# Optimization experiments

Hardware: AMD Instinct MI355X
Metric: run time of the kernel (lower is better)

The kernel has to match this reference:

```python
import jax, jax.numpy as jnp
import numpy as np

N_HEAD = 32
HEAD_DIM = 32  # must equal N_HEAD due to the module's einsum index reuse
N_EMBD = N_HEAD * HEAD_DIM
VOCAB = 32000
B, T = 2, 64
TEMP_MIN = 0.1


def setup_inputs() -> dict:
    key = jax.random.key(0)
    ks = jax.random.split(key, 8)
    inv = 1.0 / np.sqrt(HEAD_DIM)
    return {
        "x": jax.random.normal(ks[0], (B, T, N_EMBD), dtype=jnp.float32),
        "vocab_emb": jax.random.normal(ks[1], (VOCAB, N_EMBD), dtype=jnp.float32) * 0.02,
        "W_ffn": jax.random.normal(ks[2], (HEAD_DIM, HEAD_DIM), dtype=jnp.float32) * inv,
        "b_ffn": jnp.zeros((HEAD_DIM,), dtype=jnp.float32),
        "temps": jnp.ones((N_HEAD,), dtype=jnp.float32),
        "W_ref": jax.random.normal(ks[3], (HEAD_DIM, HEAD_DIM), dtype=jnp.float32) * inv,
        "b_ref": jnp.zeros((HEAD_DIM,), dtype=jnp.float32),
        "W_gate": jax.random.normal(ks[4], (HEAD_DIM, HEAD_DIM), dtype=jnp.float32) * inv,
        "b_gate": jnp.zeros((HEAD_DIM,), dtype=jnp.float32),
    }


def reference(x, vocab_emb, W_ffn, b_ffn, temps, W_ref, b_ref, W_gate, b_gate):
    Bs, Ts, C = x.shape
    # per-head channel decomposition: (B*T, n_head, head_dim)
    xc = x.reshape(Bs * Ts, N_HEAD, HEAD_DIM)
    # channel_ffns: shared Linear over the head_dim axis (torch Linear: x @ W.T + b)
    ffn = jnp.einsum('bnh,dh->bnd', xc, W_ffn) + b_ffn
    # vocab channels: (n_head, vocab, head_dim)
    vc = vocab_emb.reshape(VOCAB, N_HEAD, HEAD_DIM).transpose(1, 0, 2)
    temps_c = jnp.clip(temps, TEMP_MIN, None)[None, :, None]

    def vocab_project(q):
        # faithful to torch: einsum('bnh,hvd->bnv') contracts q's head_dim
        # against vc's HEAD axis and sums over d as well (requires head_dim == n_head)
        logits = jnp.einsum('bnh,hvd->bnv', q, vc)
        w = jax.nn.softmax(logits / temps_c, axis=-1)  # (B*T, n_head, vocab)
        return jnp.einsum('bnv,hvd->bnh', w, vc)

    vocab_out = vocab_project(ffn)  # (B*T, n_head, head_dim)

    # refinement stage (use_vocab_refinement=True)
    refinement = jnp.tanh(jnp.einsum('bnh,dh->bnd', xc, W_ref) + b_ref)
    gate = jax.nn.sigmoid(jnp.einsum('bnh,dh->bnd', xc, W_gate) + b_gate)
    refined = vocab_out * (1.0 - gate) + refinement * gate
    vocab_out = vocab_project(refined)

    # dropout p=0 (eval) -> identity
    return vocab_out.reshape(Bs, Ts, C)
```

## Files before the change

### kernel.cpp

```cpp
#include <hip/hip_runtime.h>
#include <hip/hip_bf16.h>
#include <cstdint>

typedef unsigned int uint;
typedef unsigned short ushort_t;

typedef __attribute__((ext_vector_type(8))) short short8;
typedef __attribute__((ext_vector_type(4))) short short4_t;
typedef __attribute__((ext_vector_type(4))) float float4_t;

#define NEMBD 1024
#define VOCAB 32000
#define LOG2E 1.4426950408889634f

__device__ __forceinline__ ushort_t f2bf_rne(float f) {
    uint u = __float_as_uint(f);
    u += 0x7fffu + ((u >> 16) & 1u);
    return (ushort_t)(u >> 16);
}

__global__ void k_build_st(const float* __restrict__ ve, ushort_t* __restrict__ ST) {
    int v = blockIdx.x;
    int t = threadIdx.x;
    const float4* row = (const float4*)(ve + (size_t)v * NEMBD);
    float4 f = row[t];
    float s = f.x + f.y + f.z + f.w;
    s += __shfl_down(s, 4, 8);
    s += __shfl_down(s, 2, 8);
    s += __shfl_down(s, 1, 8);
    if ((t & 7) == 0) ST[v * 32 + (t >> 3)] = f2bf_rne(s);
}

__global__ void k_build_s2(const ushort_t* __restrict__ ST, ushort_t* __restrict__ S2) {
    int tid = blockIdx.x * 256 + threadIdx.x;
    int l = tid & 63, f = (tid >> 6) & 1, c = tid >> 7;
    int quad = l >> 4, lo = l & 15;
    uint w[4];
    #pragma unroll
    for (int t = 0; t < 2; t++) {
        #pragma unroll
        for (int jj = 0; jj < 2; jj++) {
            ushort_t v0 = ST[(c * 32 + t * 16 + quad * 4 + jj * 2 + 0) * 32 + f * 16 + lo];
            ushort_t v1 = ST[(c * 32 + t * 16 + quad * 4 + jj * 2 + 1) * 32 + f * 16 + lo];
            w[t * 2 + jj] = (uint)v0 | ((uint)v1 << 16);
        }
    }
    uint4* dst = (uint4*)S2;
    dst[tid] = make_uint4(w[0], w[1], w[2], w[3]);
}

__global__ void k_q1(const float* __restrict__ x, const float* __restrict__ W,
                     const float* __restrict__ b, const float* __restrict__ temps,
                     ushort_t* __restrict__ q1) {
    int tid = blockIdx.x * 256 + threadIdx.x;
    int i = tid >> 5, d = tid & 31, n = i & 31;
    const float* xr = x + i * 32;
    float s = b[d];
    #pragma unroll
    for (int h = 0; h < 32; h++) s += xr[h] * W[d * 32 + h];
    q1[tid] = f2bf_rne(s * (LOG2E / fmaxf(temps[n], 0.1f)));
}

__launch_bounds__(256, 4)
__global__ void k_proj(const ushort_t* __restrict__ ST, const ushort_t* __restrict__ S2,
                       const ushort_t* __restrict__ q, float* __restrict__ pN,
                       float* __restrict__ pD) {
    int g = blockIdx.x >> 4, p = blockIdx.x & 15;
    int wave = threadIdx.x >> 6, lane = threadIdx.x & 63;
    int quad = lane >> 4, lo = lane & 15;

    short8 qf[4];
    #pragma unroll
    for (int s = 0; s < 4; s++)
        qf[s] = *(const short8*)(q + ((g * 64 + s * 16 + lo) * 32 + quad * 8));

    float4_t pv0[4], pv1[4];
    float dsum[4];
    #pragma unroll
    for (int s = 0; s < 4; s++) {
        pv0[s] = (float4_t){0.f, 0.f, 0.f, 0.f};
        pv1[s] = (float4_t){0.f, 0.f, 0.f, 0.f};
        dsum[s] = 0.f;
    }
    const float4_t zero4 = (float4_t){0.f, 0.f, 0.f, 0.f};

    int start = (p * 125) >> 1, end = ((p + 1) * 125) >> 1;
    for (int k = start + wave; k < end; k += 4) {
        const ushort_t* pa = ST + ((k * 32 + lo) * 32 + quad * 8);
        short8 a0 = *(const short8*)pa;
        short8 a1 = *(const short8*)(pa + 512);
        const ushort_t* pb = S2 + ((size_t)(k * 2) * 64 + lane) * 8;
        short8 sb0 = *(const short8*)pb;
        short8 sb1 = *(const short8*)(pb + 512);
        short4_t b00 = {sb0[0], sb0[1], sb0[2], sb0[3]};
        short4_t b01 = {sb0[4], sb0[5], sb0[6], sb0[7]};
        short4_t b10 = {sb1[0], sb1[1], sb1[2], sb1[3]};
        short4_t b11 = {sb1[4], sb1[5], sb1[6], sb1[7]};

        #pragma unroll
        for (int s = 0; s < 4; s++) {
            float4_t l0 = __builtin_amdgcn_mfma_f32_16x16x32_bf16(a0, qf[s], zero4, 0, 0, 0);
            float4_t l1 = __builtin_amdgcn_mfma_f32_16x16x32_bf16(a1, qf[s], zero4, 0, 0, 0);
            float e0 = __builtin_amdgcn_exp2f(l0[0]);
            float e1 = __builtin_amdgcn_exp2f(l0[1]);
            float e2 = __builtin_amdgcn_exp2f(l0[2]);
            float e3 = __builtin_amdgcn_exp2f(l0[3]);
            float f0 = __builtin_amdgcn_exp2f(l1[0]);
            float f1 = __builtin_amdgcn_exp2f(l1[1]);
            float f2 = __builtin_amdgcn_exp2f(l1[2]);
            float f3 = __builtin_amdgcn_exp2f(l1[3]);
            uint u0 = __builtin_amdgcn_perm(__float_as_uint(e1), __float_as_uint(e0), 0x07060302u);
            uint u1 = __builtin_amdgcn_perm(__float_as_uint(e3), __float_as_uint(e2), 0x07060302u);
            uint u2 = __builtin_amdgcn_perm(__float_as_uint(f1), __float_as_uint(f0), 0x07060302u);
            uint u3 = __builtin_amdgcn_perm(__float_as_uint(f3), __float_as_uint(f2), 0x07060302u);
            dsum[s] += __uint_as_float(u0 << 16) + __uint_as_float(u0 & 0xffff0000u)
                     + __uint_as_float(u1 << 16) + __uint_as_float(u1 & 0xffff0000u)
                     + __uint_as_float(u2 << 16) + __uint_as_float(u2 & 0xffff0000u)
                     + __uint_as_float(u3 << 16) + __uint_as_float(u3 & 0xffff0000u);
            union { uint u[2]; short4_t s4; } c0, c1;
            c0.u[0] = u0; c0.u[1] = u1;
            c1.u[0] = u2; c1.u[1] = u3;
            short4_t P0 = c0.s4, P1 = c1.s4;
            pv0[s] = __builtin_amdgcn_mfma_f32_16x16x16bf16_1k(P0, b00, pv0[s], 0, 0, 0);
            pv0[s] = __builtin_amdgcn_mfma_f32_16x16x16bf16_1k(P1, b01, pv0[s], 0, 0, 0);
            pv1[s] = __builtin_amdgcn_mfma_f32_16x16x16bf16_1k(P0, b10, pv1[s], 0, 0, 0);
            pv1[s] = __builtin_amdgcn_mfma_f32_16x16x16bf16_1k(P1, b11, pv1[s], 0, 0, 0);
        }
    }

    #pragma unroll
    for (int s = 0; s < 4; s++) {
        dsum[s] += __shfl_xor(dsum[s], 16, 64);
        dsum[s] += __shfl_xor(dsum[s], 32, 64);
    }

    __shared__ float red[4][64][9];
    int gp = blockIdx.x;
    for (int s = 0; s < 4; s++) {
        #pragma unroll
        for (int r = 0; r < 4; r++) {
            red[wave][lane][r]     = pv0[s][r];
            red[wave][lane][4 + r] = pv1[s][r];
        }
        red[wave][lane][8] = dsum[s];
        __syncthreads();
        if (wave == 0) {
            #pragma unroll
            for (int r = 0; r < 4; r++) {
                float n0 = 0.f, n1 = 0.f;
                #pragma unroll
                for (int w = 0; w < 4; w++) {
                    n0 += red[w][lane][r];
                    n1 += red[w][lane][4 + r];
                }
                int ql = s * 16 + quad * 4 + r;
                pN[((size_t)gp * 64 + ql) * 32 + lo]      = n0;
                pN[((size_t)gp * 64 + ql) * 32 + 16 + lo] = n1;
            }
            if (quad == 0) {
                float dd = red[0][lane][8] + red[1][lane][8] + red[2][lane][8] + red[3][lane][8];
                pD[gp * 64 + s * 16 + lo] = dd;
            }
        }
        __syncthreads();
    }
}

__global__ void k_refine(const float* __restrict__ pN, const float* __restrict__ pD,
                         const float* __restrict__ x,
                         const float* __restrict__ Wr, const float* __restrict__ br,
                         const float* __restrict__ Wg, const float* __restrict__ bg,
                         const float* __restrict__ temps, ushort_t* __restrict__ q2) {
    int tid = blockIdx.x * 256 + threadIdx.x;
    int i = tid >> 5, h = tid & 31, n = i & 31;
    int g = i >> 6, ql = i & 63;
    float N = 0.f, D = 0.f;
    #pragma unroll
    for (int p = 0; p < 16; p++) {
        N += pN[((size_t)(g * 16 + p) * 64 + ql) * 32 + h];
        D += pD[(g * 16 + p) * 64 + ql];
    }
    float vo = N / D;
    const float* xr = x + i * 32;
    float sr = br[h], sg = bg[h];
    #pragma unroll
    for (int h2 = 0; h2 < 32; h2++) {
        sr += xr[h2] * Wr[h * 32 + h2];
        sg += xr[h2] * Wg[h * 32 + h2];
    }
    float ref  = tanhf(sr);
    float gate = 1.f / (1.f + __expf(-sg));
    float refined = vo * (1.f - gate) + ref * gate;
    q2[tid] = f2bf_rne(refined * (LOG2E / fmaxf(temps[n], 0.1f)));
}

__global__ void k_final(const float* __restrict__ pN, const float* __restrict__ pD,
                        float* __restrict__ out) {
    int tid = blockIdx.x * 256 + threadIdx.x;
    int i = tid >> 5, h = tid & 31;
    int g = i >> 6, ql = i & 63;
    float N = 0.f, D = 0.f;
    #pragma unroll
    for (int p = 0; p < 16; p++) {
        N += pN[((size_t)(g * 16 + p) * 64 + ql) * 32 + h];
        D += pD[(g * 16 + p) * 64 + ql];
    }
    out[tid] = N / D;
}

extern "C" void kernel_launch(void* const* d_in, const int* in_sizes, int n_in,
                              void* d_out, int out_size, void* d_ws, size_t ws_size,
                              hipStream_t stream) {
    const float* x     = (const float*)d_in[0];
    const float* ve    = (const float*)d_in[1];
    const float* Wf    = (const float*)d_in[2];
    const float* bf    = (const float*)d_in[3];
    const float* temps = (const float*)d_in[4];
    const float* Wr    = (const float*)d_in[5];
    const float* br    = (const float*)d_in[6];
    const float* Wg    = (const float*)d_in[7];
    const float* bg    = (const float*)d_in[8];
    float* out = (float*)d_out;

    char* ws = (char*)d_ws;
    ushort_t* ST = (ushort_t*)ws;
    ushort_t* S2 = (ushort_t*)(ws + 2048000);
    ushort_t* q1 = (ushort_t*)(ws + 4096000);
    ushort_t* q2 = (ushort_t*)(ws + 4096000 + 262144);
    float* pN = (float*)(ws + 4096000 + 2 * 262144);
    float* pD = (float*)(ws + 4096000 + 2 * 262144 + 8388608);

    k_build_st<<<dim3(VOCAB), dim3(256), 0, stream>>>(ve, ST);
    k_build_s2<<<dim3(500), dim3(256), 0, stream>>>(ST, S2);
    k_q1<<<dim3(512), dim3(256), 0, stream>>>(x, Wf, bf, temps, q1);
    k_proj<<<dim3(1024), dim3(256), 0, stream>>>(ST, S2, q1, pN, pD);
    k_refine<<<dim3(512), dim3(256), 0, stream>>>(pN, pD, x, Wr, br, Wg, bg, temps, q2);
    k_proj<<<dim3(1024), dim3(256), 0, stream>>>(ST, S2, q2, pN, pD);
    k_final<<<dim3(512), dim3(256), 0, stream>>>(pN, pD, out);
}
```

Baseline: 266.4 us.

## Fuse vocab build kernels and fold q-projection and refinement into projection kernels

Merges the two vocabulary preprocessing kernels into one block-per-32-rows kernel that builds both the ST and swizzled S2 layouts through shared memory. It also fuses the q1 projection into the first projection kernel and the refinement/gate step into the second, computing each block's 64 query rows into LDS. The aim is to cut kernel launches and the global round trips for q1/q2, and to remove the extra ST reread. In exchange, each of the 16 blocks sharing a query group recomputes the same small prologue, and the second stage now needs double-buffered partial arrays.

```diff
diff --git a/kernel.cpp b/kernel.cpp
--- a/kernel.cpp
+++ b/kernel.cpp
@@ -19,60 +19,80 @@
     return (ushort_t)(u >> 16);
 }
 
-__global__ void k_build_st(const float* __restrict__ ve, ushort_t* __restrict__ ST) {
-    int v = blockIdx.x;
+__global__ void k_build(const float* __restrict__ ve, ushort_t* __restrict__ ST,
+                        ushort_t* __restrict__ S2) {
+    int blk = blockIdx.x;
     int t = threadIdx.x;
-    const float4* row = (const float4*)(ve + (size_t)v * NEMBD);
-    float4 f = row[t];
-    float s = f.x + f.y + f.z + f.w;
-    s += __shfl_down(s, 4, 8);
-    s += __shfl_down(s, 2, 8);
-    s += __shfl_down(s, 1, 8);
-    if ((t & 7) == 0) ST[v * 32 + (t >> 3)] = f2bf_rne(s);
-}
-
-__global__ void k_build_s2(const ushort_t* __restrict__ ST, ushort_t* __restrict__ S2) {
-    int tid = blockIdx.x * 256 + threadIdx.x;
-    int l = tid & 63, f = (tid >> 6) & 1, c = tid >> 7;
-    int quad = l >> 4, lo = l & 15;
-    uint w[4];
-    #pragma unroll
-    for (int t = 0; t < 2; t++) {
-        #pragma unroll
-        for (int jj = 0; jj < 2; jj++) {
-            ushort_t v0 = ST[(c * 32 + t * 16 + quad * 4 + jj * 2 + 0) * 32 + f * 16 + lo];
-            ushort_t v1 = ST[(c * 32 + t * 16 + quad * 4 + jj * 2 + 1) * 32 + f * 16 + lo];
-            w[t * 2 + jj] = (uint)v0 | ((uint)v1 << 16);
-        }
-    }
-    uint4* dst = (uint4*)S2;
-    dst[tid] = make_uint4(w[0], w[1], w[2], w[3]);
-}
-
-__global__ void k_q1(const float* __restrict__ x, const float* __restrict__ W,
-                     const float* __restrict__ b, const float* __restrict__ temps,
-                     ushort_t* __restrict__ q1) {
-    int tid = blockIdx.x * 256 + threadIdx.x;
-    int i = tid >> 5, d = tid & 31, n = i & 31;
-    const float* xr = x + i * 32;
-    float s = b[d];
-    #pragma unroll
-    for (int h = 0; h < 32; h++) s += xr[h] * W[d * 32 + h];
-    q1[tid] = f2bf_rne(s * (LOG2E / fmaxf(temps[n], 0.1f)));
+    int r = t >> 5, h = t & 31;
+    const float4* src = (const float4*)(ve + ((size_t)(blk * 32 + r)) * NEMBD + h * 32);
+    float s = 0.f;
+    #pragma unroll
+    for (int j = 0; j < 8; j++) {
+        float4 f = src[j];
+        s += f.x + f.y + f.z + f.w;
+    }
+    __shared__ __align__(16) ushort_t sm[1024];
+    sm[r * 32 + h] = f2bf_rne(s);
+    __syncthreads();
+    if (t < 128) {
+        ((uint4*)(ST + blk * 1024))[t] = ((const uint4*)sm)[t];
+    } else if (t < 256) {
+        int tt = t - 128;
+        int l = tt & 63, f = tt >> 6;
+        int quad = l >> 4, lo = l & 15;
+        uint w[4];
+        #pragma unroll
+        for (int t2 = 0; t2 < 2; t2++) {
+            #pragma unroll
+            for (int jj = 0; jj < 2; jj++) {
+                ushort_t v0 = sm[(t2 * 16 + quad * 4 + jj * 2 + 0) * 32 + f * 16 + lo];
+                ushort_t v1 = sm[(t2 * 16 + quad * 4 + jj * 2 + 1) * 32 + f * 16 + lo];
+                w[t2 * 2 + jj] = (uint)v0 | ((uint)v1 << 16);
+            }
+        }
+        ((uint4*)(S2 + blk * 1024))[tt] = make_uint4(w[0], w[1], w[2], w[3]);
+    }
 }
 
 __launch_bounds__(256, 4)
-__global__ void k_proj(const ushort_t* __restrict__ ST, const ushort_t* __restrict__ S2,
-                       const ushort_t* __restrict__ q, float* __restrict__ pN,
-                       float* __restrict__ pD) {
+__global__ void k_proj1(const ushort_t* __restrict__ ST, const ushort_t* __restrict__ S2,
+                        const float* __restrict__ x, const float* __restrict__ Wf,
+                        const float* __restrict__ bfn, const float* __restrict__ temps,
+                        float* __restrict__ pN, float* __restrict__ pD) {
+    __shared__ __align__(16) ushort_t qs[64 * 32];
+    __shared__ float red[4][64][9];
     int g = blockIdx.x >> 4, p = blockIdx.x & 15;
-    int wave = threadIdx.x >> 6, lane = threadIdx.x & 63;
+    int t = threadIdx.x;
+    int wave = t >> 6, lane = t & 63;
     int quad = lane >> 4, lo = lane & 15;
 
+    {
+        int r = t >> 2, c4 = t & 3;
+        int i = g * 64 + r, n = i & 31;
+        float sc = LOG2E / fmaxf(temps[n], 0.1f);
+        const float4* xv4 = (const float4*)(x + (size_t)i * 32);
+        float4 xv[8];
+        #pragma unroll
+        for (int j = 0; j < 8; j++) xv[j] = xv4[j];
+        #pragma unroll
+        for (int jj = 0; jj < 8; jj++) {
+            int d = c4 * 8 + jj;
+            const float4* wr = (const float4*)(Wf + d * 32);
+            float s = bfn[d];
+            #pragma unroll
+            for (int j2 = 0; j2 < 8; j2++) {
+                float4 w = wr[j2], xx = xv[j2];
+                s += xx.x * w.x + xx.y * w.y + xx.z * w.z + xx.w * w.w;
+            }
+            qs[r * 32 + d] = f2bf_rne(s * sc);
+        }
+    }
+    __syncthreads();
+
     short8 qf[4];
     #pragma unroll
     for (int s = 0; s < 4; s++)
-        qf[s] = *(const short8*)(q + ((g * 64 + s * 16 + lo) * 32 + quad * 8));
+        qf[s] = *(const short8*)(qs + (s * 16 + lo) * 32 + quad * 8);
 
     float4_t pv0[4], pv1[4];
     float dsum[4];
@@ -134,7 +154,6 @@
         dsum[s] += __shfl_xor(dsum[s], 32, 64);
     }
 
-    __shared__ float red[4][64][9];
     int gp = blockIdx.x;
     for (int s = 0; s < 4; s++) {
         #pragma unroll
@@ -166,32 +185,161 @@
     }
 }
 
-__global__ void k_refine(const float* __restrict__ pN, const float* __restrict__ pD,
-                         const float* __restrict__ x,
-                         const float* __restrict__ Wr, const float* __restrict__ br,
-                         const float* __restrict__ Wg, const float* __restrict__ bg,
-                         const float* __restrict__ temps, ushort_t* __restrict__ q2) {
-    int tid = blockIdx.x * 256 + threadIdx.x;
-    int i = tid >> 5, h = tid & 31, n = i & 31;
-    int g = i >> 6, ql = i & 63;
-    float N = 0.f, D = 0.f;
-    #pragma unroll
-    for (int p = 0; p < 16; p++) {
-        N += pN[((size_t)(g * 16 + p) * 64 + ql) * 32 + h];
-        D += pD[(g * 16 + p) * 64 + ql];
-    }
-    float vo = N / D;
-    const float* xr = x + i * 32;
-    float sr = br[h], sg = bg[h];
-    #pragma unroll
-    for (int h2 = 0; h2 < 32; h2++) {
-        sr += xr[h2] * Wr[h * 32 + h2];
-        sg += xr[h2] * Wg[h * 32 + h2];
-    }
-    float ref  = tanhf(sr);
-    float gate = 1.f / (1.f + __expf(-sg));
-    float refined = vo * (1.f - gate) + ref * gate;
-    q2[tid] = f2bf_rne(refined * (LOG2E / fmaxf(temps[n], 0.1f)));
+__launch_bounds__(256, 4)
+__global__ void k_proj2(const ushort_t* __restrict__ ST, const ushort_t* __restrict__ S2,
+                        const float* __restrict__ pNa, const float* __restrict__ pDa,
+                        const float* __restrict__ x,
+                        const float* __restrict__ Wr, const float* __restrict__ br,
+                        const float* __restrict__ Wg, const float* __restrict__ bg,
+                        const float* __restrict__ temps,
+                        float* __restrict__ pN, float* __restrict__ pD) {
+    __shared__ __align__(16) ushort_t qs[64 * 32];
+    __shared__ float red[4][64][9];
+    int g = blockIdx.x >> 4, p = blockIdx.x & 15;
+    int t = threadIdx.x;
+    int wave = t >> 6, lane = t & 63;
+    int quad = lane >> 4, lo = lane & 15;
+
+    {
+        int r = t >> 2, c4 = t & 3;
+        int i = g * 64 + r, n = i & 31;
+        float sc = LOG2E / fmaxf(temps[n], 0.1f);
+        float4 N0 = make_float4(0.f, 0.f, 0.f, 0.f);
+        float4 N1 = make_float4(0.f, 0.f, 0.f, 0.f);
+        float D = 0.f;
+        #pragma unroll
+        for (int pp = 0; pp < 16; pp++) {
+            const float* base = pNa + (((size_t)(g * 16 + pp) * 64 + r) * 32 + c4 * 8);
+            float4 a = *(const float4*)base;
+            float4 b = *(const float4*)(base + 4);
+            N0.x += a.x; N0.y += a.y; N0.z += a.z; N0.w += a.w;
+            N1.x += b.x; N1.y += b.y; N1.z += b.z; N1.w += b.w;
+            D += pDa[(g * 16 + pp) * 64 + r];
+        }
+        float invD = 1.0f / D;
+        float vo[8] = {N0.x * invD, N0.y * invD, N0.z * invD, N0.w * invD,
+                       N1.x * invD, N1.y * invD, N1.z * invD, N1.w * invD};
+        const float4* xv4 = (const float4*)(x + (size_t)i * 32);
+        float4 xv[8];
+        #pragma unroll
+        for (int j = 0; j < 8; j++) xv[j] = xv4[j];
+        #pragma unroll
+        for (int jj = 0; jj < 8; jj++) {
+            int d = c4 * 8 + jj;
+            const float4* wrr = (const float4*)(Wr + d * 32);
+            const float4* wgg = (const float4*)(Wg + d * 32);
+            float sr = br[d], sg = bg[d];
+            #pragma unroll
+            for (int j2 = 0; j2 < 8; j2++) {
+                float4 w1 = wrr[j2], w2 = wgg[j2], xx = xv[j2];
+                sr += xx.x * w1.x + xx.y * w1.y + xx.z * w1.z + xx.w * w1.w;
+                sg += xx.x * w2.x + xx.y * w2.y + xx.z * w2.z + xx.w * w2.w;
+            }
+            sr = fminf(fmaxf(sr, -20.f), 20.f);
+            float tE = __builtin_amdgcn_exp2f(sr * (2.f * LOG2E));
+            float th = (tE - 1.f) * __builtin_amdgcn_rcpf(tE + 1.f);
+            float gE = __builtin_amdgcn_exp2f(fminf(fmaxf(-sg, -20.f), 20.f) * LOG2E);
+            float gate = __builtin_amdgcn_rcpf(1.f + gE);
+            float refined = vo[jj] + gate * (th - vo[jj]);
+            qs[r * 32 + d] = f2bf_rne(refined * sc);
+        }
+    }
+    __syncthreads();
+
+    short8 qf[4];
+    #pragma unroll
+    for (int s = 0; s < 4; s++)
+        qf[s] = *(const short8*)(qs + (s * 16 + lo) * 32 + quad * 8);
+
+    float4_t pv0[4], pv1[4];
+    float dsum[4];
+    #pragma unroll
+    for (int s = 0; s < 4; s++) {
+        pv0[s] = (float4_t){0.f, 0.f, 0.f, 0.f};
+        pv1[s] = (float4_t){0.f, 0.f, 0.f, 0.f};
+        dsum[s] = 0.f;
+    }
+    const float4_t zero4 = (float4_t){0.f, 0.f, 0.f, 0.f};
+
+    int start = (p * 125) >> 1, end = ((p + 1) * 125) >> 1;
+    for (int k = start + wave; k < end; k += 4) {
+        const ushort_t* pa = ST + ((k * 32 + lo) * 32 + quad * 8);
+        short8 a0 = *(const short8*)pa;
+        short8 a1 = *(const short8*)(pa + 512);
+        const ushort_t* pb = S2 + ((size_t)(k * 2) * 64 + lane) * 8;
+        short8 sb0 = *(const short8*)pb;
+        short8 sb1 = *(const short8*)(pb + 512);
+        short4_t b00 = {sb0[0], sb0[1], sb0[2], sb0[3]};
+        short4_t b01 = {sb0[4], sb0[5], sb0[6], sb0[7]};
+        short4_t b10 = {sb1[0], sb1[1], sb1[2], sb1[3]};
+        short4_t b11 = {sb1[4], sb1[5], sb1[6], sb1[7]};
+
+        #pragma unroll
+        for (int s = 0; s < 4; s++) {
+            float4_t l0 = __builtin_amdgcn_mfma_f32_16x16x32_bf16(a0, qf[s], zero4, 0, 0, 0);
+            float4_t l1 = __builtin_amdgcn_mfma_f32_16x16x32_bf16(a1, qf[s], zero4, 0, 0, 0);
+            float e0 = __builtin_amdgcn_exp2f(l0[0]);
+            float e1 = __builtin_amdgcn_exp2f(l0[1]);
+            float e2 = __builtin_amdgcn_exp2f(l0[2]);
+            float e3 = __builtin_amdgcn_exp2f(l0[3]);
+            float f0 = __builtin_amdgcn_exp2f(l1[0]);
+            float f1 = __builtin_amdgcn_exp2f(l1[1]);
+            float f2 = __builtin_amdgcn_exp2f(l1[2]);
+            float f3 = __builtin_amdgcn_exp2f(l1[3]);
+            uint u0 = __builtin_amdgcn_perm(__float_as_uint(e1), __float_as_uint(e0), 0x07060302u);
+            uint u1 = __builtin_amdgcn_perm(__float_as_uint(e3), __float_as_uint(e2), 0x07060302u);
+            uint u2 = __builtin_amdgcn_perm(__float_as_uint(f1), __float_as_uint(f0), 0x07060302u);
+            uint u3 = __builtin_amdgcn_perm(__float_as_uint(f3), __float_as_uint(f2), 0x07060302u);
+            dsum[s] += __uint_as_float(u0 << 16) + __uint_as_float(u0 & 0xffff0000u)
+                     + __uint_as_float(u1 << 16) + __uint_as_float(u1 & 0xffff0000u)
+                     + __uint_as_float(u2 << 16) + __uint_as_float(u2 & 0xffff0000u)
+                     + __uint_as_float(u3 << 16) + __uint_as_float(u3 & 0xffff0000u);
+            union { uint u[2]; short4_t s4; } c0, c1;
+            c0.u[0] = u0; c0.u[1] = u1;
+            c1.u[0] = u2; c1.u[1] = u3;
+            short4_t P0 = c0.s4, P1 = c1.s4;
+            pv0[s] = __builtin_amdgcn_mfma_f32_16x16x16bf16_1k(P0, b00, pv0[s], 0, 0, 0);
+            pv0[s] = __builtin_amdgcn_mfma_f32_16x16x16bf16_1k(P1, b01, pv0[s], 0, 0, 0);
+            pv1[s] = __builtin_amdgcn_mfma_f32_16x16x16bf16_1k(P0, b10, pv1[s], 0, 0, 0);
+            pv1[s] = __builtin_amdgcn_mfma_f32_16x16x16bf16_1k(P1, b11, pv1[s], 0, 0, 0);
+        }
+    }
+
+    #pragma unroll
+    for (int s = 0; s < 4; s++) {
+        dsum[s] += __shfl_xor(dsum[s], 16, 64);
+        dsum[s] += __shfl_xor(dsum[s], 32, 64);
+    }
+
+    int gp = blockIdx.x;
+    for (int s = 0; s < 4; s++) {
+        #pragma unroll
+        for (int r = 0; r < 4; r++) {
+            red[wave][lane][r]     = pv0[s][r];
+            red[wave][lane][4 + r] = pv1[s][r];
+        }
+        red[wave][lane][8] = dsum[s];
+        __syncthreads();
+        if (wave == 0) {
+            #pragma unroll
+            for (int r = 0; r < 4; r++) {
+                float n0 = 0.f, n1 = 0.f;
+                #pragma unroll
+                for (int w = 0; w < 4; w++) {
+                    n0 += red[w][lane][r];
+                    n1 += red[w][lane][4 + r];
+                }
+                int ql = s * 16 + quad * 4 + r;
+                pN[((size_t)gp * 64 + ql) * 32 + lo]      = n0;
+                pN[((size_t)gp * 64 + ql) * 32 + 16 + lo] = n1;
+            }
+            if (quad == 0) {
+                float dd = red[0][lane][8] + red[1][lane][8] + red[2][lane][8] + red[3][lane][8];
+                pD[gp * 64 + s * 16 + lo] = dd;
+            }
+        }
+        __syncthreads();
+    }
 }
 
 __global__ void k_final(const float* __restrict__ pN, const float* __restrict__ pD,
@@ -214,7 +362,7 @@
     const float* x     = (const float*)d_in[0];
     const float* ve    = (const float*)d_in[1];
     const float* Wf    = (const float*)d_in[2];
-    const float* bf    = (const float*)d_in[3];
+    const float* bfn   = (const float*)d_in[3];
     const float* temps = (const float*)d_in[4];
     const float* Wr    = (const float*)d_in[5];
     const float* br    = (const float*)d_in[6];
@@ -223,18 +371,16 @@
     float* out = (float*)d_out;
 
     char* ws = (char*)d_ws;
-    ushort_t* ST = (ushort_t*)ws;
-    ushort_t* S2 = (ushort_t*)(ws + 2048000);
-    ushort_t* q1 = (ushort_t*)(ws + 4096000);
-    ushort_t* q2 = (ushort_t*)(ws + 4096000 + 262144);
-    float* pN = (float*)(ws + 4096000 + 2 * 262144);
-    float* pD = (float*)(ws + 4096000 + 2 * 262144 + 8388608);
-
-    k_build_st<<<dim3(VOCAB), dim3(256), 0, stream>>>(ve, ST);
-    k_build_s2<<<dim3(500), dim3(256), 0, stream>>>(ST, S2);
-    k_q1<<<dim3(512), dim3(256), 0, stream>>>(x, Wf, bf, temps, q1);
-    k_proj<<<dim3(1024), dim3(256), 0, stream>>>(ST, S2, q1, pN, pD);
-    k_refine<<<dim3(512), dim3(256), 0, stream>>>(pN, pD, x, Wr, br, Wg, bg, temps, q2);
-    k_proj<<<dim3(1024), dim3(256), 0, stream>>>(ST, S2, q2, pN, pD);
-    k_final<<<dim3(512), dim3(256), 0, stream>>>(pN, pD, out);
-}
+    ushort_t* ST  = (ushort_t*)ws;
+    ushort_t* S2  = (ushort_t*)(ws + 2048000);
+    float* pNa = (float*)(ws + 4096000);
+    float* pDa = (float*)(ws + 4096000 + 8388608);
+    float* pNb = (float*)(ws + 4096000 + 8388608 + 262144);
+    float* pDb = (float*)(ws + 4096000 + 2 * 8388608 + 262144);
+
+    k_build<<<dim3(1000), dim3(1024), 0, stream>>>(ve, ST, S2);
+    k_proj1<<<dim3(1024), dim3(256), 0, stream>>>(ST, S2, x, Wf, bfn, temps, pNa, pDa);
+    k_proj2<<<dim3(1024), dim3(256), 0, stream>>>(ST, S2, pNa, pDa, x, Wr, br, Wg, bg,
+                                                  temps, pNb, pDb);
+    k_final<<<dim3(512), dim3(256), 0, stream>>>(pNb, pDb, out);
+}
```

New measurement: 343.8 us. +29.0%, slower.

## Stage vocab tiles in LDS shared across waves and split vocab finer

Applied to the files above, without the earlier changes.

The projection kernel now has all four waves share each vocab chunk. A new pack kernel pre-lays the chunks out, and they are double-buffered through LDS. Each wave owns one 16-row query slice instead of all four, which removes the cross-wave LDS reduction at the end. The vocab split goes from 16 to 32 partitions, so the grid doubles and the reduce kernels sum twice as many partials. This trades register pressure and redundant global loads for extra barriers, more partial-sum traffic and an extra packed copy of the table.

```diff
diff --git a/kernel.cpp b/kernel.cpp
--- a/kernel.cpp
+++ b/kernel.cpp
@@ -31,22 +31,31 @@
     if ((t & 7) == 0) ST[v * 32 + (t >> 3)] = f2bf_rne(s);
 }
 
-__global__ void k_build_s2(const ushort_t* __restrict__ ST, ushort_t* __restrict__ S2) {
-    int tid = blockIdx.x * 256 + threadIdx.x;
-    int l = tid & 63, f = (tid >> 6) & 1, c = tid >> 7;
-    int quad = l >> 4, lo = l & 15;
-    uint w[4];
-    #pragma unroll
-    for (int t = 0; t < 2; t++) {
+__global__ void k_pack(const ushort_t* __restrict__ ST, ushort_t* __restrict__ SA,
+                       ushort_t* __restrict__ S2) {
+    int c = blockIdx.x;
+    int t = threadIdx.x;
+    if (t < 128) {
+        int tile = t >> 6, lane = t & 63;
+        int quad = lane >> 4, lo = lane & 15;
+        uint4 d = *(const uint4*)(ST + ((size_t)(c * 32 + tile * 16 + lo)) * 32 + quad * 8);
+        ((uint4*)SA)[c * 128 + t] = d;
+    } else {
+        int tt = t - 128;
+        int f = tt >> 6, l = tt & 63;
+        int quad = l >> 4, lo = l & 15;
+        uint w[4];
         #pragma unroll
-        for (int jj = 0; jj < 2; jj++) {
-            ushort_t v0 = ST[(c * 32 + t * 16 + quad * 4 + jj * 2 + 0) * 32 + f * 16 + lo];
-            ushort_t v1 = ST[(c * 32 + t * 16 + quad * 4 + jj * 2 + 1) * 32 + f * 16 + lo];
-            w[t * 2 + jj] = (uint)v0 | ((uint)v1 << 16);
-        }
-    }
-    uint4* dst = (uint4*)S2;
-    dst[tid] = make_uint4(w[0], w[1], w[2], w[3]);
+        for (int t2 = 0; t2 < 2; t2++) {
+            #pragma unroll
+            for (int jj = 0; jj < 2; jj++) {
+                ushort_t v0 = ST[(c * 32 + t2 * 16 + quad * 4 + jj * 2 + 0) * 32 + f * 16 + lo];
+                ushort_t v1 = ST[(c * 32 + t2 * 16 + quad * 4 + jj * 2 + 1) * 32 + f * 16 + lo];
+                w[t2 * 2 + jj] = (uint)v0 | ((uint)v1 << 16);
+            }
+        }
+        ((uint4*)S2)[c * 128 + tt] = make_uint4(w[0], w[1], w[2], w[3]);
+    }
 }
 
 __global__ void k_q1(const float* __restrict__ x, const float* __restrict__ W,
@@ -61,46 +70,65 @@
     q1[tid] = f2bf_rne(s * (LOG2E / fmaxf(temps[n], 0.1f)));
 }
 
-__launch_bounds__(256, 4)
-__global__ void k_proj(const ushort_t* __restrict__ ST, const ushort_t* __restrict__ S2,
+__launch_bounds__(256, 8)
+__global__ void k_proj(const ushort_t* __restrict__ SA, const ushort_t* __restrict__ S2,
                        const ushort_t* __restrict__ q, float* __restrict__ pN,
                        float* __restrict__ pD) {
-    int g = blockIdx.x >> 4, p = blockIdx.x & 15;
-    int wave = threadIdx.x >> 6, lane = threadIdx.x & 63;
+    __shared__ ushort_t buf[2][2][2048];
+    int g = blockIdx.x >> 5, p = blockIdx.x & 31;
+    int w = threadIdx.x >> 6, lane = threadIdx.x & 63;
     int quad = lane >> 4, lo = lane & 15;
 
-    short8 qf[4];
-    #pragma unroll
-    for (int s = 0; s < 4; s++)
-        qf[s] = *(const short8*)(q + ((g * 64 + s * 16 + lo) * 32 + quad * 8));
-
-    float4_t pv0[4], pv1[4];
-    float dsum[4];
-    #pragma unroll
-    for (int s = 0; s < 4; s++) {
-        pv0[s] = (float4_t){0.f, 0.f, 0.f, 0.f};
-        pv1[s] = (float4_t){0.f, 0.f, 0.f, 0.f};
-        dsum[s] = 0.f;
-    }
+    short8 qf = *(const short8*)(q + ((g * 64 + w * 16 + lo) * 32 + quad * 8));
+
+    float4_t pv0 = (float4_t){0.f, 0.f, 0.f, 0.f};
+    float4_t pv1 = (float4_t){0.f, 0.f, 0.f, 0.f};
+    float dsum = 0.f;
     const float4_t zero4 = (float4_t){0.f, 0.f, 0.f, 0.f};
 
-    int start = (p * 125) >> 1, end = ((p + 1) * 125) >> 1;
-    for (int k = start + wave; k < end; k += 4) {
-        const ushort_t* pa = ST + ((k * 32 + lo) * 32 + quad * 8);
-        short8 a0 = *(const short8*)pa;
-        short8 a1 = *(const short8*)(pa + 512);
-        const ushort_t* pb = S2 + ((size_t)(k * 2) * 64 + lane) * 8;
-        short8 sb0 = *(const short8*)pb;
-        short8 sb1 = *(const short8*)(pb + 512);
-        short4_t b00 = {sb0[0], sb0[1], sb0[2], sb0[3]};
-        short4_t b01 = {sb0[4], sb0[5], sb0[6], sb0[7]};
-        short4_t b10 = {sb1[0], sb1[1], sb1[2], sb1[3]};
-        short4_t b11 = {sb1[4], sb1[5], sb1[6], sb1[7]};
-
-        #pragma unroll
-        for (int s = 0; s < 4; s++) {
-            float4_t l0 = __builtin_amdgcn_mfma_f32_16x16x32_bf16(a0, qf[s], zero4, 0, 0, 0);
-            float4_t l1 = __builtin_amdgcn_mfma_f32_16x16x32_bf16(a1, qf[s], zero4, 0, 0, 0);
+    int start = (p * 125) >> 2, end = ((p + 1) * 125) >> 2;
+
+    {
+        int c = start + (w >> 1);
+        if (c < end) {
+            const ushort_t* src = ((w & 1) ? S2 : SA) + (size_t)c * 1024;
+            uint4 d0 = *(const uint4*)(src + lane * 8);
+            uint4 d1 = *(const uint4*)(src + 512 + lane * 8);
+            uint4* dst = (uint4*)(&buf[0][w >> 1][(w & 1) * 1024]);
+            dst[lane] = d0;
+            dst[64 + lane] = d1;
+        }
+    }
+    __syncthreads();
+
+    int ngrp = (end - start + 1) >> 1;
+    for (int grp = 0; grp < ngrp; grp++) {
+        int cur = grp & 1;
+        int cn = start + (grp + 1) * 2 + (w >> 1);
+        if (cn < end) {
+            const ushort_t* src = ((w & 1) ? S2 : SA) + (size_t)cn * 1024;
+            uint4 d0 = *(const uint4*)(src + lane * 8);
+            uint4 d1 = *(const uint4*)(src + 512 + lane * 8);
+            uint4* dst = (uint4*)(&buf[cur ^ 1][w >> 1][(w & 1) * 1024]);
+            dst[lane] = d0;
+            dst[64 + lane] = d1;
+        }
+        int c0 = start + grp * 2;
+        int jend = (end - c0 < 2) ? (end - c0) : 2;
+        for (int j = 0; j < jend; j++) {
+            const ushort_t* sa = &buf[cur][j][0];
+            const ushort_t* s2 = &buf[cur][j][1024];
+            short8 a0 = *(const short8*)(sa + lane * 8);
+            short8 a1 = *(const short8*)(sa + 512 + lane * 8);
+            short8 sb0 = *(const short8*)(s2 + lane * 8);
+            short8 sb1 = *(const short8*)(s2 + 512 + lane * 8);
+            short4_t b00 = {sb0[0], sb0[1], sb0[2], sb0[3]};
+            short4_t b01 = {sb0[4], sb0[5], sb0[6], sb0[7]};
+            short4_t b10 = {sb1[0], sb1[1], sb1[2], sb1[3]};
+            short4_t b11 = {sb1[4], sb1[5], sb1[6], sb1[7]};
+
+            float4_t l0 = __builtin_amdgcn_mfma_f32_16x16x32_bf16(a0, qf, zero4, 0, 0, 0);
+            float4_t l1 = __builtin_amdgcn_mfma_f32_16x16x32_bf16(a1, qf, zero4, 0, 0, 0);
             float e0 = __builtin_amdgcn_exp2f(l0[0]);
             float e1 = __builtin_amdgcn_exp2f(l0[1]);
             float e2 = __builtin_amdgcn_exp2f(l0[2]);
@@ -113,57 +141,33 @@
             uint u1 = __builtin_amdgcn_perm(__float_as_uint(e3), __float_as_uint(e2), 0x07060302u);
             uint u2 = __builtin_amdgcn_perm(__float_as_uint(f1), __float_as_uint(f0), 0x07060302u);
             uint u3 = __builtin_amdgcn_perm(__float_as_uint(f3), __float_as_uint(f2), 0x07060302u);
-            dsum[s] += __uint_as_float(u0 << 16) + __uint_as_float(u0 & 0xffff0000u)
-                     + __uint_as_float(u1 << 16) + __uint_as_float(u1 & 0xffff0000u)
-                     + __uint_as_float(u2 << 16) + __uint_as_float(u2 & 0xffff0000u)
-                     + __uint_as_float(u3 << 16) + __uint_as_float(u3 & 0xffff0000u);
-            union { uint u[2]; short4_t s4; } c0, c1;
-            c0.u[0] = u0; c0.u[1] = u1;
-            c1.u[0] = u2; c1.u[1] = u3;
-            short4_t P0 = c0.s4, P1 = c1.s4;
-            pv0[s] = __builtin_amdgcn_mfma_f32_16x16x16bf16_1k(P0, b00, pv0[s], 0, 0, 0);
-            pv0[s] = __builtin_amdgcn_mfma_f32_16x16x16bf16_1k(P1, b01, pv0[s], 0, 0, 0);
-            pv1[s] = __builtin_amdgcn_mfma_f32_16x16x16bf16_1k(P0, b10, pv1[s], 0, 0, 0);
-            pv1[s] = __builtin_amdgcn_mfma_f32_16x16x16bf16_1k(P1, b11, pv1[s], 0, 0, 0);
-        }
-    }
-
-    #pragma unroll
-    for (int s = 0; s < 4; s++) {
-        dsum[s] += __shfl_xor(dsum[s], 16, 64);
-        dsum[s] += __shfl_xor(dsum[s], 32, 64);
-    }
-
-    __shared__ float red[4][64][9];
+            dsum += __uint_as_float(u0 << 16) + __uint_as_float(u0 & 0xffff0000u)
+                  + __uint_as_float(u1 << 16) + __uint_as_float(u1 & 0xffff0000u)
+                  + __uint_as_float(u2 << 16) + __uint_as_float(u2 & 0xffff0000u)
+                  + __uint_as_float(u3 << 16) + __uint_as_float(u3 & 0xffff0000u);
+            union { uint u[2]; short4_t s4; } c0u, c1u;
+            c0u.u[0] = u0; c0u.u[1] = u1;
+            c1u.u[0] = u2; c1u.u[1] = u3;
+            short4_t P0 = c0u.s4, P1 = c1u.s4;
+            pv0 = __builtin_amdgcn_mfma_f32_16x16x16bf16_1k(P0, b00, pv0, 0, 0, 0);
+            pv0 = __builtin_amdgcn_mfma_f32_16x16x16bf16_1k(P1, b01, pv0, 0, 0, 0);
+            pv1 = __builtin_amdgcn_mfma_f32_16x16x16bf16_1k(P0, b10, pv1, 0, 0, 0);
+            pv1 = __builtin_amdgcn_mfma_f32_16x16x16bf16_1k(P1, b11, pv1, 0, 0, 0);
+        }
+        __syncthreads();
+    }
+
+    dsum += __shfl_xor(dsum, 16, 64);
+    dsum += __shfl_xor(dsum, 32, 64);
+
     int gp = blockIdx.x;
-    for (int s = 0; s < 4; s++) {
-        #pragma unroll
-        for (int r = 0; r < 4; r++) {
-            red[wave][lane][r]     = pv0[s][r];
-            red[wave][lane][4 + r] = pv1[s][r];
-        }
-        red[wave][lane][8] = dsum[s];
-        __syncthreads();
-        if (wave == 0) {
-            #pragma unroll
-            for (int r = 0; r < 4; r++) {
-                float n0 = 0.f, n1 = 0.f;
-                #pragma unroll
-                for (int w = 0; w < 4; w++) {
-                    n0 += red[w][lane][r];
-                    n1 += red[w][lane][4 + r];
-                }
-                int ql = s * 16 + quad * 4 + r;
-                pN[((size_t)gp * 64 + ql) * 32 + lo]      = n0;
-                pN[((size_t)gp * 64 + ql) * 32 + 16 + lo] = n1;
-            }
-            if (quad == 0) {
-                float dd = red[0][lane][8] + red[1][lane][8] + red[2][lane][8] + red[3][lane][8];
-                pD[gp * 64 + s * 16 + lo] = dd;
-            }
-        }
-        __syncthreads();
-    }
+    #pragma unroll
+    for (int r = 0; r < 4; r++) {
+        int ql = w * 16 + quad * 4 + r;
+        pN[((size_t)gp * 64 + ql) * 32 + lo]      = pv0[r];
+        pN[((size_t)gp * 64 + ql) * 32 + 16 + lo] = pv1[r];
+    }
+    if (quad == 0) pD[gp * 64 + w * 16 + lo] = dsum;
 }
 
 __global__ void k_refine(const float* __restrict__ pN, const float* __restrict__ pD,
@@ -176,9 +180,9 @@
     int g = i >> 6, ql = i & 63;
     float N = 0.f, D = 0.f;
     #pragma unroll
-    for (int p = 0; p < 16; p++) {
-        N += pN[((size_t)(g * 16 + p) * 64 + ql) * 32 + h];
-        D += pD[(g * 16 + p) * 64 + ql];
+    for (int p = 0; p < 32; p++) {
+        N += pN[((size_t)(g * 32 + p) * 64 + ql) * 32 + h];
+        D += pD[(g * 32 + p) * 64 + ql];
     }
     float vo = N / D;
     const float* xr = x + i * 32;
@@ -201,9 +205,9 @@
     int g = i >> 6, ql = i & 63;
     float N = 0.f, D = 0.f;
     #pragma unroll
-    for (int p = 0; p < 16; p++) {
-        N += pN[((size_t)(g * 16 + p) * 64 + ql) * 32 + h];
-        D += pD[(g * 16 + p) * 64 + ql];
+    for (int p = 0; p < 32; p++) {
+        N += pN[((size_t)(g * 32 + p) * 64 + ql) * 32 + h];
+        D += pD[(g * 32 + p) * 64 + ql];
     }
     out[tid] = N / D;
 }
@@ -214,7 +218,7 @@
     const float* x     = (const float*)d_in[0];
     const float* ve    = (const float*)d_in[1];
     const float* Wf    = (const float*)d_in[2];
-    const float* bf    = (const float*)d_in[3];
+    const float* bfn   = (const float*)d_in[3];
     const float* temps = (const float*)d_in[4];
     const float* Wr    = (const float*)d_in[5];
     const float* br    = (const float*)d_in[6];
@@ -224,17 +228,21 @@
 
     char* ws = (char*)d_ws;
     ushort_t* ST = (ushort_t*)ws;
-    ushort_t* S2 = (ushort_t*)(ws + 2048000);
-    ushort_t* q1 = (ushort_t*)(ws + 4096000);
-    ushort_t* q2 = (ushort_t*)(ws + 4096000 + 262144);
-    float* pN = (float*)(ws + 4096000 + 2 * 262144);
-    float* pD = (float*)(ws + 4096000 + 2 * 262144 + 8388608);
+    ushort_t* SA = (ushort_t*)(ws + 2048000);
+    ushort_t* S2 = (ushort_t*)(ws + 4096000);
+    ushort_t* q1 = (ushort_t*)(ws + 6144000);
+    ushort_t* q2 = (ushort_t*)(ws + 6144000 + 262144);
+    char* base = ws + 6144000 + 2 * 262144;
+    float* pNa = (float*)base;
+    float* pDa = (float*)(base + 16777216);
+    float* pNb = (float*)(base + 16777216 + 524288);
+    float* pDb = (float*)(base + 2 * 16777216 + 524288);
 
     k_build_st<<<dim3(VOCAB), dim3(256), 0, stream>>>(ve, ST);
-    k_build_s2<<<dim3(500), dim3(256), 0, stream>>>(ST, S2);
-    k_q1<<<dim3(512), dim3(256), 0, stream>>>(x, Wf, bf, temps, q1);
-    k_proj<<<dim3(1024), dim3(256), 0, stream>>>(ST, S2, q1, pN, pD);
-    k_refine<<<dim3(512), dim3(256), 0, stream>>>(pN, pD, x, Wr, br, Wg, bg, temps, q2);
-    k_proj<<<dim3(1024), dim3(256), 0, stream>>>(ST, S2, q2, pN, pD);
-    k_final<<<dim3(512), dim3(256), 0, stream>>>(pN, pD, out);
-}
+    k_pack<<<dim3(1000), dim3(256), 0, stream>>>(ST, SA, S2);
+    k_q1<<<dim3(512), dim3(256), 0, stream>>>(x, Wf, bfn, temps, q1);
+    k_proj<<<dim3(2048), dim3(256), 0, stream>>>(SA, S2, q1, pNa, pDa);
+    k_refine<<<dim3(512), dim3(256), 0, stream>>>(pNa, pDa, x, Wr, br, Wg, bg, temps, q2);
+    k_proj<<<dim3(2048), dim3(256), 0, stream>>>(SA, S2, q2, pNb, pDb);
+    k_final<<<dim3(512), dim3(256), 0, stream>>>(pNb, pDb, out);
+}
```

New measurement: 276.4 us. 1.04x slower.
